# Optimization experiments

Measured on AMD Instinct MI355X. Metric: run time of the kernel, lower is better.

The kernel has to match this reference:

```python
import jax, jax.numpy as jnp
import numpy as np

ORIENTATIONS = 9
CELL = (8, 8)
BLOCK = (3, 3)
EPS = 1e-5  # skimage L2 block-norm epsilon


def _hog_features(x):
    # transform_sqrt=True (gamma compression)
    img = jnp.sqrt(x)
    H, W = img.shape
    # skimage _hog_channel_gradient: central differences, zero at borders
    g_row = jnp.zeros_like(img).at[1:-1, :].set(img[2:, :] - img[:-2, :])
    g_col = jnp.zeros_like(img).at[:, 1:-1].set(img[:, 2:] - img[:, :-2])
    mag = jnp.hypot(g_row, g_col)
    # orientation in degrees, folded to [0, 180)
    ori = jnp.rad2deg(jnp.arctan2(g_row, g_col)) % 180.0

    cr, cc = CELL
    ncr, ncc = H // cr, W // cc
    mag_c = mag[: ncr * cr, : ncc * cc]
    ori_c = ori[: ncr * cr, : ncc * cc]
    unit = 180.0 / ORIENTATIONS

    # hard binning (skimage uses no interpolation); small fixed loop over bins
    hists = []
    for b in range(ORIENTATIONS):
        sel = (ori_c >= b * unit) & (ori_c < (b + 1) * unit)
        m = jnp.where(sel, mag_c, 0.0)
        # per-cell mean of selected magnitudes: [ncr, ncc]
        cell = m.reshape(ncr, cr, ncc, cc).mean(axis=(1, 3))
        hists.append(cell)
    hist = jnp.stack(hists, axis=-1)  # [ncr, ncc, orientations]

    br_n, bc_n = BLOCK
    nbr, nbc = ncr - br_n + 1, ncc - bc_n + 1
    # overlapping blocks: [nbr, nbc, br_n, bc_n, orientations]
    blocks = jnp.stack(
        [jnp.stack([hist[i : i + nbr, j : j + nbc] for j in range(bc_n)], axis=2)
         for i in range(br_n)],
        axis=2,
    )
    # L2 block normalization: b / sqrt(sum(b^2) + eps^2)
    denom = jnp.sqrt(jnp.sum(blocks * blocks, axis=(2, 3, 4), keepdims=True) + EPS ** 2)
    normalized = blocks / denom
    return normalized.reshape(-1)  # feature_vector=True


def setup_inputs() -> dict:
    key = jax.random.key(0)
    x = jax.random.uniform(key, (4096, 4096), dtype=jnp.float32)
    return {"x": x}


def reference(x):
    return _hog_features(x)
```

## Files before the change

### kernel.cpp

```cpp
#include <hip/hip_runtime.h>
#include <math.h>

#define H 4096
#define W 4096
#define NC 512
#define NB 510
#define ORI 9
#define NCELLS (NC * NC)
#define NOUT (NB * NB * 81)

__device__ __forceinline__ float fdlibm_atanf(float x) {
#pragma clang fp contract(off)
    const float one = 1.0f;
    const float aT0  = (float) 3.33333333333329318027e-01;
    const float aT1  = (float)-1.99999999998764832476e-01;
    const float aT2  = (float) 1.42857142725034663711e-01;
    const float aT3  = (float)-1.11111104054623557880e-01;
    const float aT4  = (float) 9.09088713343650656196e-02;
    const float aT5  = (float)-7.69187620504482999495e-02;
    const float aT6  = (float) 6.66107313738753120669e-02;
    const float aT7  = (float)-5.83357013379057348645e-02;
    const float aT8  = (float) 4.97687799461593236017e-02;
    const float aT9  = (float)-3.65315727442169155270e-02;
    const float aT10 = (float) 1.62858201153657823623e-02;
    const float athi[4] = {4.6364760399e-01f, 7.8539812565e-01f,
                           9.8279368877e-01f, 1.5707962513e+00f};
    const float atlo[4] = {5.0121582440e-09f, 3.7748947079e-08f,
                           3.4473217170e-08f, 7.5497894159e-08f};
    int hx = __float_as_int(x);
    int ix = hx & 0x7fffffff;
    int id;
    if (ix >= 0x4c800000) {
        if (ix > 0x7f800000) return x + x;
        float r = athi[3] + atlo[3];
        return (hx > 0) ? r : -r;
    }
    if (ix < 0x3ee00000) {
        if (ix < 0x31000000) return x;
        id = -1;
    } else {
        x = fabsf(x);
        if (ix < 0x3f980000) {
            if (ix < 0x3f300000) { id = 0; x = (2.0f * x - one) / (2.0f + x); }
            else                 { id = 1; x = (x - one) / (x + one); }
        } else {
            if (ix < 0x401c0000) { id = 2; x = (x - 1.5f) / (one + 1.5f * x); }
            else                 { id = 3; x = -1.0f / x; }
        }
    }
    float z = x * x;
    float w = z * z;
    float s1 = z * (aT0 + w * (aT2 + w * (aT4 + w * (aT6 + w * (aT8 + w * aT10)))));
    float s2 = w * (aT1 + w * (aT3 + w * (aT5 + w * (aT7 + w * aT9))));
    if (id < 0) return x - x * (s1 + s2);
    z = athi[id] - ((x * (s1 + s2) - atlo[id]) - x);
    return (hx < 0) ? -z : z;
}

__device__ __forceinline__ float fdlibm_atan2f(float y, float x) {
#pragma clang fp contract(off)
    const float tiny   = 1.0e-30f;
    const float pi     = 3.1415927410e+00f;
    const float pi_lo  = -8.7422776573e-08f;
    const float pi_o_2 = 1.5707963705e+00f;
    int hx = __float_as_int(x), ix = hx & 0x7fffffff;
    int hy = __float_as_int(y), iy = hy & 0x7fffffff;
    if (hx == 0x3f800000) return fdlibm_atanf(y);
    int m = ((hy >> 31) & 1) | ((hx >> 30) & 2);
    if (iy == 0) {
        switch (m) {
            case 0: case 1: return y;
            case 2: return pi + tiny;
            default: return -pi - tiny;
        }
    }
    if (ix == 0) return (hy < 0) ? -pi_o_2 - tiny : pi_o_2 + tiny;
    int k = (iy - ix) >> 23;
    float z;
    if (k > 26) { z = pi_o_2 + 0.5f * pi_lo; m &= 1; }
    else if (k < -26 && hx < 0) z = 0.0f;
    else z = fdlibm_atanf(fabsf(y / x));
    switch (m) {
        case 0: return z;
        case 1: return -z;
        case 2: return pi - (z - pi_lo);
        default: return (z - pi_lo) - pi;
    }
}

__device__ __forceinline__ int slow_bin_px(const float* __restrict__ x,
                                           int grow, int gc,
                                           bool row_ok, bool col_ok) {
#pragma clang fp contract(off)
    float gy = 0.0f, gx = 0.0f;
    if (row_ok)
        gy = sqrtf(x[(grow + 1) * W + gc]) - sqrtf(x[(grow - 1) * W + gc]);
    if (col_ok)
        gx = sqrtf(x[grow * W + gc + 1]) - sqrtf(x[grow * W + gc - 1]);
    float ang = fdlibm_atan2f(gy, gx);
    const float RAD2DEG = (float)(180.0 / 3.14159265358979323846264338328);
    float deg = ang * RAD2DEG;
    float m = fmodf(deg, 180.0f);
    if (m < 0.0f) m += 180.0f;
    int bin = (int)(m / 20.0f);
    if (bin < 9 && m >= (float)((bin + 1) * 20)) bin++;
    else if (bin > 0 && m < (float)(bin * 20)) bin--;
    return bin;
}

#define T20 ((float) 0.36397023426620236135)
#define T40 ((float) 0.83909963117728001176)
#define T60 ((float) 1.73205080756887729353)
#define T80 ((float) 5.67128181961771110517)

__device__ __forceinline__ float dpp_add8(float v) {
    int t = __builtin_amdgcn_update_dpp(0, __float_as_int(v), 0xB1, 0xF, 0xF, true);
    v += __int_as_float(t);
    t = __builtin_amdgcn_update_dpp(0, __float_as_int(v), 0x4E, 0xF, 0xF, true);
    v += __int_as_float(t);
    t = __builtin_amdgcn_update_dpp(0, __float_as_int(v), 0x141, 0xF, 0xF, true);
    v += __int_as_float(t);
    return v;
}

__global__ __launch_bounds__(256, 4) void hog_hist(const float* __restrict__ x,
                                                   float* __restrict__ hist,
                                                   float* __restrict__ q) {
    int t = threadIdx.x;
    int w = t >> 6, lane = t & 63;
    int wid = blockIdx.x * 4 + w;
    int crow = wid >> 6;
    int strip = wid & 63;
    int gc = (strip << 6) + lane;

    int r0 = (crow << 3) - 1;
    int rtop = (r0 < 0) ? 0 : r0;
    int rbot = (r0 + 9 > H - 1) ? (H - 1) : (r0 + 9);
    int gcl = (gc == 0) ? 0 : gc - 1;
    int gcr = (gc == W - 1) ? (W - 1) : gc + 1;

    float s[10], sl[8], sr[8];
    s[0] = x[rtop * W + gc];
#pragma unroll
    for (int k = 1; k < 9; ++k) s[k] = x[(r0 + k) * W + gc];
    s[9] = x[rbot * W + gc];
#pragma unroll
    for (int j = 0; j < 8; ++j) {
        int grow = (crow << 3) + j;
        sl[j] = x[grow * W + gcl];
        sr[j] = x[grow * W + gcr];
    }
#pragma unroll
    for (int k = 0; k < 10; ++k) s[k] = __builtin_amdgcn_sqrtf(s[k]);
#pragma unroll
    for (int j = 0; j < 8; ++j) {
        sl[j] = __builtin_amdgcn_sqrtf(sl[j]);
        sr[j] = __builtin_amdgcn_sqrtf(sr[j]);
    }

    bool col_ok = (gc >= 1) && (gc <= W - 2);
    float SA = 0.f, TA1 = 0.f, TA2 = 0.f, TA3 = 0.f, TA4 = 0.f;
    float SB = 0.f, TB1 = 0.f, TB2 = 0.f, TB3 = 0.f, TB4 = 0.f;
    unsigned gbits = 0;

#pragma unroll
    for (int j = 0; j < 8; ++j) {
        int grow = (crow << 3) + j;
        bool row_ok = (grow >= 1) && (grow <= H - 2);
        float gy = row_ok ? (s[j + 2] - s[j]) : 0.0f;
        float gx = col_ok ? (sr[j] - sl[j]) : 0.0f;

        float a = fabsf(gy), b = fabsf(gx);
        float d1 = fmaf(b, -T20, a);
        float d2 = fmaf(b, -T40, a);
        float d3 = fmaf(b, -T60, a);
        float d4 = fmaf(b, -T80, a);

        float cm = fminf(fminf(fabsf(d1), fabsf(d2)),
                         fminf(fminf(fabsf(d3), fabsf(d4)), a));
        bool guard = cm < fmaf(1e-5f, a + b, 4e-6f);
        if (guard) gbits |= (1u << j);

        bool opp = ((__float_as_int(gy) ^ __float_as_int(gx)) < 0);
        float mag = __builtin_amdgcn_sqrtf(fmaf(gy, gy, gx * gx));
        float magA = (!opp && !guard) ? mag : 0.0f;
        float magB = (opp && !guard) ? mag : 0.0f;

        SA  += magA;
        TA1 += (d1 > 0.0f) ? magA : 0.0f;
        TA2 += (d2 > 0.0f) ? magA : 0.0f;
        TA3 += (d3 > 0.0f) ? magA : 0.0f;
        TA4 += (d4 > 0.0f) ? magA : 0.0f;
        SB  += magB;
        TB1 += (d1 > 0.0f) ? magB : 0.0f;
        TB2 += (d2 > 0.0f) ? magB : 0.0f;
        TB3 += (d3 > 0.0f) ? magB : 0.0f;
        TB4 += (d4 > 0.0f) ? magB : 0.0f;
    }

    float bb[9];
    bb[0] = SA - TA1;  bb[1] = TA1 - TA2;  bb[2] = TA2 - TA3;  bb[3] = TA3 - TA4;
    bb[4] = TA4 + TB4;
    bb[5] = TB3 - TB4; bb[6] = TB2 - TB3;  bb[7] = TB1 - TB2;  bb[8] = SB - TB1;

    if (__any(gbits != 0)) {
#pragma unroll
        for (int j = 0; j < 8; ++j) {
            if ((gbits >> j) & 1u) {
                int grow = (crow << 3) + j;
                bool row_ok = (grow >= 1) && (grow <= H - 2);
                int bin = slow_bin_px(x, grow, gc, row_ok, col_ok);
                float gy = row_ok ? (s[j + 2] - s[j]) : 0.0f;
                float gx = col_ok ? (sr[j] - sl[j]) : 0.0f;
                float mag = __builtin_amdgcn_sqrtf(fmaf(gy, gy, gx * gx));
#pragma unroll
                for (int b2 = 0; b2 < 9; ++b2) bb[b2] += (bin == b2) ? mag : 0.0f;
            }
        }
    }

#pragma unroll
    for (int b2 = 0; b2 < 9; ++b2) bb[b2] = dpp_add8(bb[b2]);

    int cell = lane >> 3;
    int k = lane & 7;
    int cbase = crow * (NC * ORI) + strip * 72 + cell * 9;
    float hv = bb[0];
#pragma unroll
    for (int b2 = 1; b2 < 8; ++b2) hv = (k == b2) ? bb[b2] : hv;
    hist[cbase + k] = hv * (1.0f / 64.0f);
    if (k == 0) {
        hist[cbase + 8] = bb[8] * (1.0f / 64.0f);
        float qq = 0.0f;
#pragma unroll
        for (int b2 = 0; b2 < 9; ++b2) {
            float h = bb[b2] * (1.0f / 64.0f);
            qq = fmaf(h, h, qq);
        }
        q[crow * NC + strip * 8 + cell] = qq;
    }
}

__global__ __launch_bounds__(256) void hog_inv(const float* __restrict__ q,
                                               float* __restrict__ inv) {
    int t = blockIdx.x * 256 + threadIdx.x;
    if (t >= NB * NB) return;
    int i = t / NB;
    int j = t - i * NB;
    float ssq = 0.0f;
#pragma unroll
    for (int bi = 0; bi < 3; ++bi)
#pragma unroll
        for (int bj = 0; bj < 3; ++bj)
            ssq += q[(i + bi) * NC + (j + bj)];
    inv[t] = 1.0f / sqrtf(ssq + 1e-10f);
}

__global__ __launch_bounds__(256) void hog_norm4(const float* __restrict__ hist,
                                                 const float* __restrict__ inv,
                                                 float4* __restrict__ out4, int n4) {
    int v = blockIdx.x * 256 + threadIdx.x;
    if (v >= n4) return;
    int k0 = v * 4;
    float r[4];
#pragma unroll
    for (int e = 0; e < 4; ++e) {
        int k = k0 + e;
        int pidx = k / 81;
        int e81 = k - pidx * 81;
        int i = pidx / NB;
        int j = pidx - i * NB;
        int bi = e81 / 27;
        int rr = e81 - bi * 27;
        int bj = rr / 9;
        int o = rr - bj * 9;
        r[e] = hist[((i + bi) * NC + (j + bj)) * ORI + o] * inv[pidx];
    }
    out4[v] = make_float4(r[0], r[1], r[2], r[3]);
}

extern "C" void kernel_launch(void* const* d_in, const int* in_sizes, int n_in,
                              void* d_out, int out_size, void* d_ws, size_t ws_size,
                              hipStream_t stream) {
    const float* x = (const float*)d_in[0];
    float* out = (float*)d_out;
    float* hist = (float*)d_ws;
    float* inv  = hist + NCELLS * ORI;
    float* q = out + (NOUT - NCELLS);

    hog_hist<<<(NC * 64) / 4, 256, 0, stream>>>(x, hist, q);
    hog_inv<<<(NB * NB + 255) / 256, 256, 0, stream>>>(q, inv);
    int n4 = out_size / 4;
    hog_norm4<<<(n4 + 255) / 256, 256, 0, stream>>>(hist, inv, (float4*)out, n4);
}
```

Measured before the change: 66.31 us.

## Process four columns per thread with float4 loads in HOG histogram kernel

Each thread in the histogram kernel now handles four adjacent pixel columns using float4 loads, so a wave covers 256 columns and the grid shrinks fourfold. Horizontal neighbours are taken from registers rather than reloaded, which cuts redundant global loads and sqrt work on halo columns. The per-cell reduction needs only one DPP step, and each lane pair writes a cell's histogram. The cost is higher register pressure, fewer waves in flight, and a guard fallback path that now reloads values from global memory.

```diff
diff --git a/kernel.cpp b/kernel.cpp
--- a/kernel.cpp
+++ b/kernel.cpp
@@ -113,14 +113,9 @@
 #define T60 ((float) 1.73205080756887729353)
 #define T80 ((float) 5.67128181961771110517)
 
-__device__ __forceinline__ float dpp_add8(float v) {
-    int t = __builtin_amdgcn_update_dpp(0, __float_as_int(v), 0xB1, 0xF, 0xF, true);
-    v += __int_as_float(t);
-    t = __builtin_amdgcn_update_dpp(0, __float_as_int(v), 0x4E, 0xF, 0xF, true);
-    v += __int_as_float(t);
-    t = __builtin_amdgcn_update_dpp(0, __float_as_int(v), 0x141, 0xF, 0xF, true);
-    v += __int_as_float(t);
-    return v;
+__device__ __forceinline__ float f4c(const float4& v, int c) {
+    switch (c) { case 0: return v.x; case 1: return v.y;
+                 case 2: return v.z; default: return v.w; }
 }
 
 __global__ __launch_bounds__(256, 4) void hog_hist(const float* __restrict__ x,
@@ -129,36 +124,45 @@
     int t = threadIdx.x;
     int w = t >> 6, lane = t & 63;
     int wid = blockIdx.x * 4 + w;
-    int crow = wid >> 6;
-    int strip = wid & 63;
-    int gc = (strip << 6) + lane;
+    int crow = wid >> 4;
+    int cs   = wid & 15;
+    int gc0  = (cs << 8) + (lane << 2);
 
     int r0 = (crow << 3) - 1;
     int rtop = (r0 < 0) ? 0 : r0;
     int rbot = (r0 + 9 > H - 1) ? (H - 1) : (r0 + 9);
-    int gcl = (gc == 0) ? 0 : gc - 1;
-    int gcr = (gc == W - 1) ? (W - 1) : gc + 1;
-
-    float s[10], sl[8], sr[8];
-    s[0] = x[rtop * W + gc];
-#pragma unroll
-    for (int k = 1; k < 9; ++k) s[k] = x[(r0 + k) * W + gc];
-    s[9] = x[rbot * W + gc];
+    int gcl = (gc0 == 0) ? 0 : gc0 - 1;
+    int gcr = (gc0 + 4 > W - 1) ? (W - 1) : gc0 + 4;
+
+    const float4* x4 = (const float4*)x;
+    int c4 = (gc0 >> 2);
+    float4 s4[10];
+    s4[0] = x4[rtop * 1024 + c4];
+#pragma unroll
+    for (int k = 1; k < 9; ++k) s4[k] = x4[(r0 + k) * 1024 + c4];
+    s4[9] = x4[rbot * 1024 + c4];
+    float sL[8], sR[8];
 #pragma unroll
     for (int j = 0; j < 8; ++j) {
         int grow = (crow << 3) + j;
-        sl[j] = x[grow * W + gcl];
-        sr[j] = x[grow * W + gcr];
-    }
-#pragma unroll
-    for (int k = 0; k < 10; ++k) s[k] = __builtin_amdgcn_sqrtf(s[k]);
+        sL[j] = x[grow * W + gcl];
+        sR[j] = x[grow * W + gcr];
+    }
+#pragma unroll
+    for (int k = 0; k < 10; ++k) {
+        s4[k].x = __builtin_amdgcn_sqrtf(s4[k].x);
+        s4[k].y = __builtin_amdgcn_sqrtf(s4[k].y);
+        s4[k].z = __builtin_amdgcn_sqrtf(s4[k].z);
+        s4[k].w = __builtin_amdgcn_sqrtf(s4[k].w);
+    }
 #pragma unroll
     for (int j = 0; j < 8; ++j) {
-        sl[j] = __builtin_amdgcn_sqrtf(sl[j]);
-        sr[j] = __builtin_amdgcn_sqrtf(sr[j]);
-    }
-
-    bool col_ok = (gc >= 1) && (gc <= W - 2);
+        sL[j] = __builtin_amdgcn_sqrtf(sL[j]);
+        sR[j] = __builtin_amdgcn_sqrtf(sR[j]);
+    }
+
+    bool okL = (gc0 >= 1);
+    bool okR = (gc0 + 3 <= W - 2);
     float SA = 0.f, TA1 = 0.f, TA2 = 0.f, TA3 = 0.f, TA4 = 0.f;
     float SB = 0.f, TB1 = 0.f, TB2 = 0.f, TB3 = 0.f, TB4 = 0.f;
     unsigned gbits = 0;
@@ -167,35 +171,40 @@
     for (int j = 0; j < 8; ++j) {
         int grow = (crow << 3) + j;
         bool row_ok = (grow >= 1) && (grow <= H - 2);
-        float gy = row_ok ? (s[j + 2] - s[j]) : 0.0f;
-        float gx = col_ok ? (sr[j] - sl[j]) : 0.0f;
-
-        float a = fabsf(gy), b = fabsf(gx);
-        float d1 = fmaf(b, -T20, a);
-        float d2 = fmaf(b, -T40, a);
-        float d3 = fmaf(b, -T60, a);
-        float d4 = fmaf(b, -T80, a);
-
-        float cm = fminf(fminf(fabsf(d1), fabsf(d2)),
-                         fminf(fminf(fabsf(d3), fabsf(d4)), a));
-        bool guard = cm < fmaf(1e-5f, a + b, 4e-6f);
-        if (guard) gbits |= (1u << j);
-
-        bool opp = ((__float_as_int(gy) ^ __float_as_int(gx)) < 0);
-        float mag = __builtin_amdgcn_sqrtf(fmaf(gy, gy, gx * gx));
-        float magA = (!opp && !guard) ? mag : 0.0f;
-        float magB = (opp && !guard) ? mag : 0.0f;
-
-        SA  += magA;
-        TA1 += (d1 > 0.0f) ? magA : 0.0f;
-        TA2 += (d2 > 0.0f) ? magA : 0.0f;
-        TA3 += (d3 > 0.0f) ? magA : 0.0f;
-        TA4 += (d4 > 0.0f) ? magA : 0.0f;
-        SB  += magB;
-        TB1 += (d1 > 0.0f) ? magB : 0.0f;
-        TB2 += (d2 > 0.0f) ? magB : 0.0f;
-        TB3 += (d3 > 0.0f) ? magB : 0.0f;
-        TB4 += (d4 > 0.0f) ? magB : 0.0f;
+#pragma unroll
+        for (int c = 0; c < 4; ++c) {
+            float gy = row_ok ? (f4c(s4[j + 2], c) - f4c(s4[j], c)) : 0.0f;
+            float left  = (c == 0) ? sL[j] : f4c(s4[j + 1], c - 1);
+            float right = (c == 3) ? sR[j] : f4c(s4[j + 1], c + 1);
+            bool col_ok = (c == 0) ? okL : ((c == 3) ? okR : true);
+            float gx = col_ok ? (right - left) : 0.0f;
+
+            float a = fabsf(gy), b = fabsf(gx);
+            float d1 = fmaf(b, -T20, a);
+            float d2 = fmaf(b, -T40, a);
+            float d3 = fmaf(b, -T60, a);
+            float d4 = fmaf(b, -T80, a);
+            float cm = fminf(fminf(fabsf(d1), fabsf(d2)),
+                             fminf(fminf(fabsf(d3), fabsf(d4)), a));
+            bool guard = cm < fmaf(1e-5f, a + b, 4e-6f);
+            if (guard) gbits |= (1u << (j * 4 + c));
+
+            bool opp = ((__float_as_int(gy) ^ __float_as_int(gx)) < 0);
+            float mag = __builtin_amdgcn_sqrtf(fmaf(gy, gy, gx * gx));
+            float magA = (!opp && !guard) ? mag : 0.0f;
+            float magB = (opp && !guard) ? mag : 0.0f;
+
+            SA  += magA;
+            TA1 += (d1 > 0.0f) ? magA : 0.0f;
+            TA2 += (d2 > 0.0f) ? magA : 0.0f;
+            TA3 += (d3 > 0.0f) ? magA : 0.0f;
+            TA4 += (d4 > 0.0f) ? magA : 0.0f;
+            SB  += magB;
+            TB1 += (d1 > 0.0f) ? magB : 0.0f;
+            TB2 += (d2 > 0.0f) ? magB : 0.0f;
+            TB3 += (d3 > 0.0f) ? magB : 0.0f;
+            TB4 += (d4 > 0.0f) ? magB : 0.0f;
+        }
     }
 
     float bb[9];
@@ -204,40 +213,51 @@
     bb[5] = TB3 - TB4; bb[6] = TB2 - TB3;  bb[7] = TB1 - TB2;  bb[8] = SB - TB1;
 
     if (__any(gbits != 0)) {
-#pragma unroll
-        for (int j = 0; j < 8; ++j) {
-            if ((gbits >> j) & 1u) {
-                int grow = (crow << 3) + j;
-                bool row_ok = (grow >= 1) && (grow <= H - 2);
-                int bin = slow_bin_px(x, grow, gc, row_ok, col_ok);
-                float gy = row_ok ? (s[j + 2] - s[j]) : 0.0f;
-                float gx = col_ok ? (sr[j] - sl[j]) : 0.0f;
-                float mag = __builtin_amdgcn_sqrtf(fmaf(gy, gy, gx * gx));
-#pragma unroll
-                for (int b2 = 0; b2 < 9; ++b2) bb[b2] += (bin == b2) ? mag : 0.0f;
-            }
-        }
-    }
-
-#pragma unroll
-    for (int b2 = 0; b2 < 9; ++b2) bb[b2] = dpp_add8(bb[b2]);
-
-    int cell = lane >> 3;
-    int k = lane & 7;
-    int cbase = crow * (NC * ORI) + strip * 72 + cell * 9;
-    float hv = bb[0];
-#pragma unroll
-    for (int b2 = 1; b2 < 8; ++b2) hv = (k == b2) ? bb[b2] : hv;
-    hist[cbase + k] = hv * (1.0f / 64.0f);
+        unsigned gb = gbits;
+        while (gb) {
+            int bpos = __ffs(gb) - 1;
+            gb &= gb - 1;
+            int j = bpos >> 2, c = bpos & 3;
+            int grow = (crow << 3) + j;
+            int gc = gc0 + c;
+            bool row_ok = (grow >= 1) && (grow <= H - 2);
+            bool col_ok = (gc >= 1) && (gc <= W - 2);
+            int bin = slow_bin_px(x, grow, gc, row_ok, col_ok);
+            float gyE = 0.0f, gxE = 0.0f;
+            if (row_ok) gyE = sqrtf(x[(grow + 1) * W + gc]) - sqrtf(x[(grow - 1) * W + gc]);
+            if (col_ok) gxE = sqrtf(x[grow * W + gc + 1]) - sqrtf(x[grow * W + gc - 1]);
+            float mag = sqrtf(fmaf(gyE, gyE, gxE * gxE));
+#pragma unroll
+            for (int b2 = 0; b2 < 9; ++b2) bb[b2] += (bin == b2) ? mag : 0.0f;
+        }
+    }
+
+#pragma unroll
+    for (int b2 = 0; b2 < 9; ++b2) {
+        int tv = __builtin_amdgcn_update_dpp(0, __float_as_int(bb[b2]),
+                                             0xB1, 0xF, 0xF, true);
+        bb[b2] += __int_as_float(tv);
+    }
+
+    int cell = lane >> 1;
+    int k = lane & 1;
+    int cbase = crow * (NC * ORI) + ((cs << 5) + cell) * 9;
+#pragma unroll
+    for (int e = 0; e < 5; ++e) {
+        float v0 = bb[e];
+        float v1 = (e < 4) ? bb[5 + e] : 0.0f;
+        float val = k ? v1 : v0;
+        int off = k ? (5 + e) : e;
+        if (!k || e < 4) hist[cbase + off] = val * (1.0f / 64.0f);
+    }
     if (k == 0) {
-        hist[cbase + 8] = bb[8] * (1.0f / 64.0f);
         float qq = 0.0f;
 #pragma unroll
         for (int b2 = 0; b2 < 9; ++b2) {
             float h = bb[b2] * (1.0f / 64.0f);
             qq = fmaf(h, h, qq);
         }
-        q[crow * NC + strip * 8 + cell] = qq;
+        q[crow * NC + (cs << 5) + cell] = qq;
     }
 }
 
@@ -288,7 +308,7 @@
     float* inv  = hist + NCELLS * ORI;
     float* q = out + (NOUT - NCELLS);
 
-    hog_hist<<<(NC * 64) / 4, 256, 0, stream>>>(x, hist, q);
+    hog_hist<<<(NC * 16) / 4, 256, 0, stream>>>(x, hist, q);
     hog_inv<<<(NB * NB + 255) / 256, 256, 0, stream>>>(q, inv);
     int n4 = out_size / 4;
     hog_norm4<<<(n4 + 255) / 256, 256, 0, stream>>>(hist, inv, (float4*)out, n4);
```

Measured after the change: 65.69 us (median of 2 runs). Within noise of the previous version (-0.9%).
